# Kernel optimization log

Hardware: AMD Instinct MI355X
Metric: run time of the kernel (lower is better)

Reference implementation:

```python
import jax, jax.numpy as jnp
import numpy as np

K = 3  # neighborhood kernel size (hard-coded by the view(B,H,W,3,3) in the source)
BIG_NEG = jnp.float32(-1e9)   # stand-in for -inf on masked neighbors (safe under softmax)
ROW_NEG = jnp.float32(-1e8)   # value used by the source for fully-occluded rows


def extract_local_patches(x, k=K):
    """x: [B,C,H,W] -> [B,C,H,W,k*k] with replicate padding (F.pad mode='replicate')."""
    p = k // 2
    xp = jnp.pad(x, ((0, 0), (0, 0), (p, p), (p, p)), mode='edge')
    B, C, H, W = x.shape
    shifts = [xp[:, :, i:i + H, j:j + W] for i in range(k) for j in range(k)]
    return jnp.stack(shifts, axis=-1)  # [B,C,H,W,k*k]


def setup_inputs() -> dict:
    key = jax.random.key(0)
    k1, k2, k3, k4 = jax.random.split(key, 4)
    B, C, H, W = 4, 640, 64, 64
    Ft = jax.random.normal(k1, (B, C, H, W), dtype=jnp.float32)
    Fwarp = jax.random.normal(k2, (B, C, H, W), dtype=jnp.float32)
    mask = jax.random.bernoulli(k3, 0.3, (B, 1, H, W)).astype(jnp.float32)
    conv_w = jax.random.normal(k4, (1, 2 * C), dtype=jnp.float32) * (1.0 / np.sqrt(2 * C))
    conv_b = jnp.zeros((1,), dtype=jnp.float32)
    return {"Ft": Ft, "Fwarp": Fwarp, "mask": mask, "conv_w": conv_w, "conv_b": conv_b}


def reference(Ft, Fwarp, mask, conv_w, conv_b):
    B, C, H, W = Ft.shape
    # 3x3 neighborhood of Fwarp: [B,C,H,W,9]
    Fp = extract_local_patches(Fwarp)
    # per-pixel dot product of Ft query with each of its 9 neighbors
    sim = jnp.einsum('bchw,bchwn->bhwn', Ft, Fp) / jnp.sqrt(jnp.float32(C))  # [B,H,W,9]
    # mask neighborhoods: [B,H,W,9]
    mp = extract_local_patches(mask)[:, 0]
    occluded = (mp == 1.0)
    sim = jnp.where(occluded, BIG_NEG, sim)
    # rows where every neighbor is occluded get a uniform large-negative row,
    # softmax'd then zeroed (matches masked_fill(-inf) -> -1e8 -> zero-out)
    valid = jnp.any(~occluded, axis=-1, keepdims=True)  # [B,H,W,1]
    sim = jnp.where(valid, sim, ROW_NEG)
    attn = jax.nn.softmax(sim, axis=-1)
    attn = jnp.where(valid, attn, 0.0)  # [B,H,W,9]
    # weighted sum over the 9 neighbors
    Fw = jnp.einsum('bchwn,bhwn->bchw', Fp, attn)  # [B,C,H,W]
    # lambda predictor: 1x1 conv + sigmoid over cat([Fwarp_weighted, Ft])
    x = jnp.concatenate([Fw, Ft], axis=1)  # [B,2C,H,W]
    lam = jax.nn.sigmoid(jnp.einsum('bihw,oi->bohw', x, conv_w) + conv_b[None, :, None, None])
    return lam * Ft + (1.0 - lam) * Fw
```

## Files before the change

kernel.cpp:

```cpp
#include <hip/hip_runtime.h>

#define B_    4
#define C_    640
#define H_    64
#define W_    64
#define NT    512
#define G_    8
#define CPG   40
#define CHALF 320

__device__ __forceinline__ void decode_bhs(int n, int& b, int& h, int& s) {
    const int xcd = n & 7;
    const int i   = n >> 3;
    h = xcd * 8 + (i & 7);
    s = (i >> 3) & 1;
    b = i >> 4;
}

__device__ __forceinline__ void row_acc(const float4 ft4, const float4 r,
                                        const int l16, float* a) {
    const float pw = __shfl_up(r.w, 1, 64);
    const float nx = __shfl_down(r.x, 1, 64);
    const float vL0 = (l16 == 0)  ? r.x : pw;
    const float vR3 = (l16 == 15) ? r.w : nx;
    a[0]  = fmaf(ft4.x, vL0, a[0]);
    a[1]  = fmaf(ft4.y, r.x, a[1]);
    a[2]  = fmaf(ft4.z, r.y, a[2]);
    a[3]  = fmaf(ft4.w, r.z, a[3]);
    a[4]  = fmaf(ft4.x, r.x, a[4]);
    a[5]  = fmaf(ft4.y, r.y, a[5]);
    a[6]  = fmaf(ft4.z, r.z, a[6]);
    a[7]  = fmaf(ft4.w, r.w, a[7]);
    a[8]  = fmaf(ft4.x, r.y, a[8]);
    a[9]  = fmaf(ft4.y, r.z, a[9]);
    a[10] = fmaf(ft4.z, r.w, a[10]);
    a[11] = fmaf(ft4.w, vR3, a[11]);
}

__device__ __forceinline__ void row_fw(const float4 r, const int l16,
                                       const float* at, const int r3, float* fwv) {
    const float pw = __shfl_up(r.w, 1, 64);
    const float nx = __shfl_down(r.x, 1, 64);
    const float vL0 = (l16 == 0)  ? r.x : pw;
    const float vR3 = (l16 == 15) ? r.w : nx;
    fwv[0] += at[0*9+r3]*vL0 + at[0*9+r3+1]*r.x + at[0*9+r3+2]*r.y;
    fwv[1] += at[1*9+r3]*r.x + at[1*9+r3+1]*r.y + at[1*9+r3+2]*r.z;
    fwv[2] += at[2*9+r3]*r.y + at[2*9+r3+1]*r.z + at[2*9+r3+2]*r.w;
    fwv[3] += at[3*9+r3]*r.z + at[3*9+r3+1]*r.w + at[3*9+r3+2]*vR3;
}

__global__ __launch_bounds__(NT, 4) void k1_sim(
    const float* __restrict__ Ft, const float* __restrict__ Fwp,
    const float* __restrict__ cw,
    float* __restrict__ simp, float* __restrict__ ptp)
{
    __shared__ float lds_cw[2 * C_];
    __shared__ float lds_sim[G_][W_][9];
    __shared__ float lds_PT[G_][4][W_];

    const int t   = threadIdx.x;
    const int l   = t & 63;
    const int g   = t >> 6;
    const int sub = l >> 4;
    const int l16 = l & 15;
    const int w0  = l16 * 4;

    int b, h, s; decode_bhs(blockIdx.x, b, h, s);
    const int hm = (h > 0) ? h - 1 : 0;
    const int hp = (h < H_ - 1) ? h + 1 : H_ - 1;
    const size_t cs = (size_t)H_ * W_;
    const int c0 = s * CHALF + g * CPG;

    for (int i = t; i < 2 * C_; i += NT) lds_cw[i] = cw[i];
    __syncthreads();

    const size_t base = (size_t)(b * C_ + c0) * H_;
    const size_t lo   = (size_t)sub * cs + w0;
    const float* ftp = Ft  + (base + h ) * W_ + lo;
    const float* q0p = Fwp + (base + hm) * W_ + lo;
    const float* q1p = Fwp + (base + h ) * W_ + lo;
    const float* q2p = Fwp + (base + hp) * W_ + lo;

    float acc[36], Pp[12], T4[4];
    #pragma unroll
    for (int i = 0; i < 36; ++i) acc[i] = 0.f;
    #pragma unroll
    for (int i = 0; i < 12; ++i) Pp[i] = 0.f;
    #pragma unroll
    for (int i = 0; i < 4; ++i) T4[i] = 0.f;

    #pragma unroll 2
    for (int k = 0; k < CPG; k += 4) {
        const size_t off = (size_t)k * cs;
        const float4 ft4 = *(const float4*)(ftp + off);
        const float4 r0  = *(const float4*)(q0p + off);
        const float4 r1  = *(const float4*)(q1p + off);
        const float4 r2  = *(const float4*)(q2p + off);
        row_acc(ft4, r0, l16, &acc[0]);
        row_acc(ft4, r1, l16, &acc[12]);
        row_acc(ft4, r2, l16, &acc[24]);
        const int c = c0 + k + sub;
        const float wF = lds_cw[c];
        const float wT = lds_cw[C_ + c];
        Pp[0] = fmaf(wF, r0.x, Pp[0]); Pp[1]  = fmaf(wF, r0.y, Pp[1]);
        Pp[2] = fmaf(wF, r0.z, Pp[2]); Pp[3]  = fmaf(wF, r0.w, Pp[3]);
        Pp[4] = fmaf(wF, r1.x, Pp[4]); Pp[5]  = fmaf(wF, r1.y, Pp[5]);
        Pp[6] = fmaf(wF, r1.z, Pp[6]); Pp[7]  = fmaf(wF, r1.w, Pp[7]);
        Pp[8] = fmaf(wF, r2.x, Pp[8]); Pp[9]  = fmaf(wF, r2.y, Pp[9]);
        Pp[10]= fmaf(wF, r2.z, Pp[10]);Pp[11] = fmaf(wF, r2.w, Pp[11]);
        T4[0] = fmaf(wT, ft4.x, T4[0]); T4[1] = fmaf(wT, ft4.y, T4[1]);
        T4[2] = fmaf(wT, ft4.z, T4[2]); T4[3] = fmaf(wT, ft4.w, T4[3]);
    }

    #pragma unroll
    for (int i = 0; i < 36; ++i) {
        acc[i] += __shfl_xor(acc[i], 16, 64);
        acc[i] += __shfl_xor(acc[i], 32, 64);
    }
    #pragma unroll
    for (int i = 0; i < 12; ++i) {
        Pp[i] += __shfl_xor(Pp[i], 16, 64);
        Pp[i] += __shfl_xor(Pp[i], 32, 64);
    }
    #pragma unroll
    for (int i = 0; i < 4; ++i) {
        T4[i] += __shfl_xor(T4[i], 16, 64);
        T4[i] += __shfl_xor(T4[i], 32, 64);
    }

    if (l < 16) {
        #pragma unroll
        for (int px = 0; px < 4; ++px) {
            #pragma unroll
            for (int r = 0; r < 3; ++r) {
                #pragma unroll
                for (int cc = 0; cc < 3; ++cc)
                    lds_sim[g][w0 + px][r * 3 + cc] = acc[r * 12 + cc * 4 + px];
                lds_PT[g][r][w0 + px] = Pp[r * 4 + px];
            }
            lds_PT[g][3][w0 + px] = T4[px];
        }
    }
    __syncthreads();

    const size_t r2i = (size_t)((b * H_ + h) * 2 + s);
    float* sp = simp + r2i * (W_ * 9);
    for (int idx = t; idx < W_ * 9; idx += NT) {
        const int ww = idx / 9, q = idx % 9;
        float v = 0.f;
        #pragma unroll
        for (int gg = 0; gg < G_; ++gg) v += lds_sim[gg][ww][q];
        sp[idx] = v;
    }
    if (t < 4 * W_) {
        const int r = t >> 6, ww = t & 63;
        float v = 0.f;
        #pragma unroll
        for (int gg = 0; gg < G_; ++gg) v += lds_PT[gg][r][ww];
        ptp[r2i * (4 * W_) + t] = v;
    }
}

__global__ __launch_bounds__(NT, 4) void k2_out(
    const float* __restrict__ Ft, const float* __restrict__ Fwp,
    const float* __restrict__ mask, const float* __restrict__ cb,
    const float* __restrict__ simp, const float* __restrict__ ptp,
    float* __restrict__ out)
{
    __shared__ float lds_msk[3][W_];
    __shared__ float lds_attn[W_][9];
    __shared__ float lds_Pf[4][W_];
    __shared__ float lds_lam[W_];

    const int t   = threadIdx.x;
    const int l   = t & 63;
    const int g   = t >> 6;
    const int sub = l >> 4;
    const int l16 = l & 15;
    const int w0  = l16 * 4;

    int b, h, s; decode_bhs(blockIdx.x, b, h, s);
    const int hm = (h > 0) ? h - 1 : 0;
    const int hp = (h < H_ - 1) ? h + 1 : H_ - 1;
    const size_t cs = (size_t)H_ * W_;
    const int c0 = s * CHALF + g * CPG;

    if (t < 3 * W_) {
        const int r = t >> 6, col = t & 63;
        const int row = (r == 0) ? hm : ((r == 1) ? h : hp);
        lds_msk[r][col] = mask[((size_t)b * H_ + row) * W_ + col];
    }
    __syncthreads();

    const size_t bh2 = (size_t)((b * H_ + h) * 2);
    const float* sp0 = simp + (bh2 + 0) * (W_ * 9);
    const float* sp1 = simp + (bh2 + 1) * (W_ * 9);
    for (int idx = t; idx < W_ * 9; idx += NT) {
        const int ww = idx / 9, q = idx % 9;
        float v = (sp0[idx] + sp1[idx]) * 0.03952847075210474f;
        const int r = q / 3, j = q % 3;
        int col = ww + j - 1;
        col = col < 0 ? 0 : (col > W_ - 1 ? W_ - 1 : col);
        if (lds_msk[r][col] == 1.0f) v = -1e9f;
        lds_attn[ww][q] = v;
    }
    if (t < 4 * W_) {
        lds_Pf[t >> 6][t & 63] =
            ptp[(bh2 + 0) * (4 * W_) + t] + ptp[(bh2 + 1) * (4 * W_) + t];
    }
    __syncthreads();

    if (t < W_) {
        float v[9];
        float mx = -3e38f;
        bool valid = false;
        #pragma unroll
        for (int q = 0; q < 9; ++q) {
            v[q] = lds_attn[t][q];
            if (v[q] > -5e8f) valid = true;
            mx = fmaxf(mx, v[q]);
        }
        float a9[9];
        if (!valid) {
            #pragma unroll
            for (int q = 0; q < 9; ++q) a9[q] = 0.f;
        } else {
            float sum = 0.f;
            #pragma unroll
            for (int q = 0; q < 9; ++q) { a9[q] = expf(v[q] - mx); sum += a9[q]; }
            const float inv = 1.f / sum;
            #pragma unroll
            for (int q = 0; q < 9; ++q) a9[q] *= inv;
        }
        #pragma unroll
        for (int q = 0; q < 9; ++q) lds_attn[t][q] = a9[q];

        float lamF = 0.f;
        #pragma unroll
        for (int r = 0; r < 3; ++r)
            #pragma unroll
            for (int j = 0; j < 3; ++j) {
                int col = t + j - 1;
                col = col < 0 ? 0 : (col > W_ - 1 ? W_ - 1 : col);
                lamF = fmaf(a9[r * 3 + j], lds_Pf[r][col], lamF);
            }
        const float d = lds_Pf[3][t] + lamF + cb[0];
        lds_lam[t] = 1.f / (1.f + expf(-d));
    }
    __syncthreads();

    float at[36];
    #pragma unroll
    for (int px = 0; px < 4; ++px)
        #pragma unroll
        for (int q = 0; q < 9; ++q) at[px * 9 + q] = lds_attn[w0 + px][q];
    float lam4[4], oml4[4];
    #pragma unroll
    for (int px = 0; px < 4; ++px) {
        lam4[px] = lds_lam[w0 + px];
        oml4[px] = 1.f - lam4[px];
    }

    const size_t base = (size_t)(b * C_ + c0) * H_;
    const size_t lo   = (size_t)sub * cs + w0;
    const float* ftp = Ft  + (base + h ) * W_ + lo;
    const float* q0p = Fwp + (base + hm) * W_ + lo;
    const float* q1p = Fwp + (base + h ) * W_ + lo;
    const float* q2p = Fwp + (base + hp) * W_ + lo;
    float* outp = out + (base + h) * W_ + lo;

    #pragma unroll 2
    for (int k = 0; k < CPG; k += 4) {
        const size_t off = (size_t)k * cs;
        const float4 ft4 = *(const float4*)(ftp + off);
        const float4 r0  = *(const float4*)(q0p + off);
        const float4 r1  = *(const float4*)(q1p + off);
        const float4 r2  = *(const float4*)(q2p + off);
        float fwv[4] = {0.f, 0.f, 0.f, 0.f};
        row_fw(r0, l16, at, 0, fwv);
        row_fw(r1, l16, at, 3, fwv);
        row_fw(r2, l16, at, 6, fwv);
        float4 o;
        o.x = lam4[0] * ft4.x + oml4[0] * fwv[0];
        o.y = lam4[1] * ft4.y + oml4[1] * fwv[1];
        o.z = lam4[2] * ft4.z + oml4[2] * fwv[2];
        o.w = lam4[3] * ft4.w + oml4[3] * fwv[3];
        *(float4*)(outp + off) = o;
    }
}

extern "C" void kernel_launch(void* const* d_in, const int* in_sizes, int n_in,
                              void* d_out, int out_size, void* d_ws, size_t ws_size,
                              hipStream_t stream) {
    const float* Ft   = (const float*)d_in[0];
    const float* Fwp  = (const float*)d_in[1];
    const float* mask = (const float*)d_in[2];
    const float* cw   = (const float*)d_in[3];
    const float* cb   = (const float*)d_in[4];
    float* out = (float*)d_out;

    float* simp = (float*)d_ws;
    float* ptp  = simp + (size_t)512 * (W_ * 9);

    dim3 grid(B_ * H_ * 2);
    dim3 block(NT);
    k1_sim<<<grid, block, 0, stream>>>(Ft, Fwp, cw, simp, ptp);
    k2_out<<<grid, block, 0, stream>>>(Ft, Fwp, mask, cb, simp, ptp, out);
}
```

Measured before the change: 47.60 us.

## Fuse similarity and output kernels with per-row atomic flag handshake

Merges the two kernels into one. The two blocks that handle a (b,h) row's channel halves exchange partial similarity sums through global memory, guarded by a per-row atomic counter and a spin-wait. This drops one kernel launch and lets the second phase reuse the Ft/Fwarp pointers, with the data likely still in cache. In exchange it adds a memset launch and 19KB of dynamic shared memory that is requested but never used, which may lower occupancy. The spin-wait deadlocks unless both partner blocks are resident at the same time, which holds only because the grid of 512 blocks fits on the device.

```diff
diff --git a/kernel.cpp b/kernel.cpp
--- a/kernel.cpp
+++ b/kernel.cpp
@@ -49,14 +49,20 @@
     fwv[3] += at[3*9+r3]*r.z + at[3*9+r3+1]*r.w + at[3*9+r3+2]*vR3;
 }
 
-__global__ __launch_bounds__(NT, 4) void k1_sim(
+__global__ __launch_bounds__(NT, 4) void nca_persist(
     const float* __restrict__ Ft, const float* __restrict__ Fwp,
-    const float* __restrict__ cw,
-    float* __restrict__ simp, float* __restrict__ ptp)
+    const float* __restrict__ mask,
+    const float* __restrict__ cw, const float* __restrict__ cb,
+    int* __restrict__ flags, float* __restrict__ simp, float* __restrict__ ptp,
+    float* __restrict__ out)
 {
     __shared__ float lds_cw[2 * C_];
+    __shared__ float lds_msk[3][W_];
     __shared__ float lds_sim[G_][W_][9];
     __shared__ float lds_PT[G_][4][W_];
+    __shared__ float lds_attn[W_][9];
+    __shared__ float lds_Pf[4][W_];
+    __shared__ float lds_lam[W_];
 
     const int t   = threadIdx.x;
     const int l   = t & 63;
@@ -66,12 +72,18 @@
     const int w0  = l16 * 4;
 
     int b, h, s; decode_bhs(blockIdx.x, b, h, s);
+    const int rowid = b * H_ + h;
     const int hm = (h > 0) ? h - 1 : 0;
     const int hp = (h < H_ - 1) ? h + 1 : H_ - 1;
     const size_t cs = (size_t)H_ * W_;
     const int c0 = s * CHALF + g * CPG;
 
     for (int i = t; i < 2 * C_; i += NT) lds_cw[i] = cw[i];
+    if (t < 3 * W_) {
+        const int r = t >> 6, col = t & 63;
+        const int row = (r == 0) ? hm : ((r == 1) ? h : hp);
+        lds_msk[r][col] = mask[((size_t)b * H_ + row) * W_ + col];
+    }
     __syncthreads();
 
     const size_t base = (size_t)(b * C_ + c0) * H_;
@@ -143,7 +155,7 @@
     }
     __syncthreads();
 
-    const size_t r2i = (size_t)((b * H_ + h) * 2 + s);
+    const size_t r2i = (size_t)(rowid * 2 + s);
     float* sp = simp + r2i * (W_ * 9);
     for (int idx = t; idx < W_ * 9; idx += NT) {
         const int ww = idx / 9, q = idx % 9;
@@ -159,40 +171,19 @@
         for (int gg = 0; gg < G_; ++gg) v += lds_PT[gg][r][ww];
         ptp[r2i * (4 * W_) + t] = v;
     }
-}
-
-__global__ __launch_bounds__(NT, 4) void k2_out(
-    const float* __restrict__ Ft, const float* __restrict__ Fwp,
-    const float* __restrict__ mask, const float* __restrict__ cb,
-    const float* __restrict__ simp, const float* __restrict__ ptp,
-    float* __restrict__ out)
-{
-    __shared__ float lds_msk[3][W_];
-    __shared__ float lds_attn[W_][9];
-    __shared__ float lds_Pf[4][W_];
-    __shared__ float lds_lam[W_];
-
-    const int t   = threadIdx.x;
-    const int l   = t & 63;
-    const int g   = t >> 6;
-    const int sub = l >> 4;
-    const int l16 = l & 15;
-    const int w0  = l16 * 4;
-
-    int b, h, s; decode_bhs(blockIdx.x, b, h, s);
-    const int hm = (h > 0) ? h - 1 : 0;
-    const int hp = (h < H_ - 1) ? h + 1 : H_ - 1;
-    const size_t cs = (size_t)H_ * W_;
-    const int c0 = s * CHALF + g * CPG;
-
-    if (t < 3 * W_) {
-        const int r = t >> 6, col = t & 63;
-        const int row = (r == 0) ? hm : ((r == 1) ? h : hp);
-        lds_msk[r][col] = mask[((size_t)b * H_ + row) * W_ + col];
-    }
-    __syncthreads();
-
-    const size_t bh2 = (size_t)((b * H_ + h) * 2);
+
+    __threadfence();
+    __syncthreads();
+    if (t == 0) {
+        atomicAdd(&flags[rowid], 1);
+        while (atomicAdd(&flags[rowid], 0) < 2) {
+            __builtin_amdgcn_s_sleep(2);
+        }
+        __threadfence();
+    }
+    __syncthreads();
+
+    const size_t bh2 = (size_t)(rowid * 2);
     const float* sp0 = simp + (bh2 + 0) * (W_ * 9);
     const float* sp1 = simp + (bh2 + 1) * (W_ * 9);
     for (int idx = t; idx < W_ * 9; idx += NT) {
@@ -261,14 +252,7 @@
         oml4[px] = 1.f - lam4[px];
     }
 
-    const size_t base = (size_t)(b * C_ + c0) * H_;
-    const size_t lo   = (size_t)sub * cs + w0;
-    const float* ftp = Ft  + (base + h ) * W_ + lo;
-    const float* q0p = Fwp + (base + hm) * W_ + lo;
-    const float* q1p = Fwp + (base + h ) * W_ + lo;
-    const float* q2p = Fwp + (base + hp) * W_ + lo;
     float* outp = out + (base + h) * W_ + lo;
-
     #pragma unroll 2
     for (int k = 0; k < CPG; k += 4) {
         const size_t off = (size_t)k * cs;
@@ -299,11 +283,14 @@
     const float* cb   = (const float*)d_in[4];
     float* out = (float*)d_out;
 
-    float* simp = (float*)d_ws;
-    float* ptp  = simp + (size_t)512 * (W_ * 9);
+    int*   flags = (int*)d_ws;
+    float* simp  = (float*)((char*)d_ws + 1024);
+    float* ptp   = simp + (size_t)512 * (W_ * 9);
+
+    hipMemsetAsync(d_ws, 0, 1024, stream);
 
     dim3 grid(B_ * H_ * 2);
     dim3 block(NT);
-    k1_sim<<<grid, block, 0, stream>>>(Ft, Fwp, cw, simp, ptp);
-    k2_out<<<grid, block, 0, stream>>>(Ft, Fwp, mask, cb, simp, ptp, out);
-}
+    nca_persist<<<grid, block, 19 * 1024, stream>>>(
+        Ft, Fwp, mask, cw, cb, flags, simp, ptp, out);
+}
```

Result: slower. 130.8 us (+174.9%).

## Fuse two kernels into one cooperative launch with grid-wide barrier

Applied to the files above, without the earlier changes.

Merges the similarity pass and the output pass into a single cooperative kernel separated by a grid sync, so the gap between two launches disappears and the same blocks reread their input rows while they may still sit in cache. Mask and conv weights are loaded once at the start. The fused kernel uses more shared memory and the grid barrier costs time, which can reduce occupancy. If the cooperative launch fails, the code falls back to the two original kernels.

```diff
diff --git a/kernel.cpp b/kernel.cpp
--- a/kernel.cpp
+++ b/kernel.cpp
@@ -1,4 +1,7 @@
 #include <hip/hip_runtime.h>
+#include <hip/hip_cooperative_groups.h>
+
+namespace cg = cooperative_groups;
 
 #define B_    4
 #define C_    640
@@ -49,38 +52,12 @@
     fwv[3] += at[3*9+r3]*r.z + at[3*9+r3+1]*r.w + at[3*9+r3+2]*vR3;
 }
 
-__global__ __launch_bounds__(NT, 4) void k1_sim(
-    const float* __restrict__ Ft, const float* __restrict__ Fwp,
-    const float* __restrict__ cw,
-    float* __restrict__ simp, float* __restrict__ ptp)
-{
-    __shared__ float lds_cw[2 * C_];
-    __shared__ float lds_sim[G_][W_][9];
-    __shared__ float lds_PT[G_][4][W_];
-
-    const int t   = threadIdx.x;
-    const int l   = t & 63;
-    const int g   = t >> 6;
-    const int sub = l >> 4;
-    const int l16 = l & 15;
-    const int w0  = l16 * 4;
-
-    int b, h, s; decode_bhs(blockIdx.x, b, h, s);
-    const int hm = (h > 0) ? h - 1 : 0;
-    const int hp = (h < H_ - 1) ? h + 1 : H_ - 1;
-    const size_t cs = (size_t)H_ * W_;
-    const int c0 = s * CHALF + g * CPG;
-
-    for (int i = t; i < 2 * C_; i += NT) lds_cw[i] = cw[i];
-    __syncthreads();
-
-    const size_t base = (size_t)(b * C_ + c0) * H_;
-    const size_t lo   = (size_t)sub * cs + w0;
-    const float* ftp = Ft  + (base + h ) * W_ + lo;
-    const float* q0p = Fwp + (base + hm) * W_ + lo;
-    const float* q1p = Fwp + (base + h ) * W_ + lo;
-    const float* q2p = Fwp + (base + hp) * W_ + lo;
-
+__device__ __forceinline__ void phase1_stream(
+    const float* ftp, const float* q0p, const float* q1p, const float* q2p,
+    const float* lds_cw, int c0, int sub, int l, int l16, int g, int w0, int t,
+    float (*lds_sim)[W_][9], float (*lds_PT)[4][W_],
+    float* simp, float* ptp, size_t r2i, size_t cs)
+{
     float acc[36], Pp[12], T4[4];
     #pragma unroll
     for (int i = 0; i < 36; ++i) acc[i] = 0.f;
@@ -143,7 +120,6 @@
     }
     __syncthreads();
 
-    const size_t r2i = (size_t)((b * H_ + h) * 2 + s);
     float* sp = simp + r2i * (W_ * 9);
     for (int idx = t; idx < W_ * 9; idx += NT) {
         const int ww = idx / 9, q = idx % 9;
@@ -161,38 +137,12 @@
     }
 }
 
-__global__ __launch_bounds__(NT, 4) void k2_out(
-    const float* __restrict__ Ft, const float* __restrict__ Fwp,
-    const float* __restrict__ mask, const float* __restrict__ cb,
-    const float* __restrict__ simp, const float* __restrict__ ptp,
-    float* __restrict__ out)
-{
-    __shared__ float lds_msk[3][W_];
-    __shared__ float lds_attn[W_][9];
-    __shared__ float lds_Pf[4][W_];
-    __shared__ float lds_lam[W_];
-
-    const int t   = threadIdx.x;
-    const int l   = t & 63;
-    const int g   = t >> 6;
-    const int sub = l >> 4;
-    const int l16 = l & 15;
-    const int w0  = l16 * 4;
-
-    int b, h, s; decode_bhs(blockIdx.x, b, h, s);
-    const int hm = (h > 0) ? h - 1 : 0;
-    const int hp = (h < H_ - 1) ? h + 1 : H_ - 1;
-    const size_t cs = (size_t)H_ * W_;
-    const int c0 = s * CHALF + g * CPG;
-
-    if (t < 3 * W_) {
-        const int r = t >> 6, col = t & 63;
-        const int row = (r == 0) ? hm : ((r == 1) ? h : hp);
-        lds_msk[r][col] = mask[((size_t)b * H_ + row) * W_ + col];
-    }
-    __syncthreads();
-
-    const size_t bh2 = (size_t)((b * H_ + h) * 2);
+__device__ __forceinline__ void phase2_out(
+    const float* ftp, const float* q0p, const float* q1p, const float* q2p,
+    float* outp, const float* simp, const float* ptp, const float* cb,
+    const float (*lds_msk)[W_], float (*lds_attn)[9], float (*lds_Pf)[W_],
+    float* lds_lam, int t, int l16, int w0, size_t bh2, size_t cs)
+{
     const float* sp0 = simp + (bh2 + 0) * (W_ * 9);
     const float* sp1 = simp + (bh2 + 1) * (W_ * 9);
     for (int idx = t; idx < W_ * 9; idx += NT) {
@@ -260,14 +210,6 @@
         lam4[px] = lds_lam[w0 + px];
         oml4[px] = 1.f - lam4[px];
     }
-
-    const size_t base = (size_t)(b * C_ + c0) * H_;
-    const size_t lo   = (size_t)sub * cs + w0;
-    const float* ftp = Ft  + (base + h ) * W_ + lo;
-    const float* q0p = Fwp + (base + hm) * W_ + lo;
-    const float* q1p = Fwp + (base + h ) * W_ + lo;
-    const float* q2p = Fwp + (base + hp) * W_ + lo;
-    float* outp = out + (base + h) * W_ + lo;
 
     #pragma unroll 2
     for (int k = 0; k < CPG; k += 4) {
@@ -289,6 +231,125 @@
     }
 }
 
+__global__ __launch_bounds__(NT, 4) void nca_coop(
+    const float* __restrict__ Ft, const float* __restrict__ Fwp,
+    const float* __restrict__ mask,
+    const float* __restrict__ cw, const float* __restrict__ cb,
+    float* __restrict__ simp, float* __restrict__ ptp,
+    float* __restrict__ out)
+{
+    __shared__ float lds_cw[2 * C_];
+    __shared__ float lds_msk[3][W_];
+    __shared__ float lds_sim[G_][W_][9];
+    __shared__ float lds_PT[G_][4][W_];
+    __shared__ float lds_attn[W_][9];
+    __shared__ float lds_Pf[4][W_];
+    __shared__ float lds_lam[W_];
+
+    const int t   = threadIdx.x;
+    const int l   = t & 63;
+    const int g   = t >> 6;
+    const int sub = l >> 4;
+    const int l16 = l & 15;
+    const int w0  = l16 * 4;
+
+    int b, h, s; decode_bhs(blockIdx.x, b, h, s);
+    const int rowid = b * H_ + h;
+    const int hm = (h > 0) ? h - 1 : 0;
+    const int hp = (h < H_ - 1) ? h + 1 : H_ - 1;
+    const size_t cs = (size_t)H_ * W_;
+    const int c0 = s * CHALF + g * CPG;
+
+    for (int i = t; i < 2 * C_; i += NT) lds_cw[i] = cw[i];
+    if (t < 3 * W_) {
+        const int r = t >> 6, col = t & 63;
+        const int row = (r == 0) ? hm : ((r == 1) ? h : hp);
+        lds_msk[r][col] = mask[((size_t)b * H_ + row) * W_ + col];
+    }
+    __syncthreads();
+
+    const size_t base = (size_t)(b * C_ + c0) * H_;
+    const size_t lo   = (size_t)sub * cs + w0;
+    const float* ftp = Ft  + (base + h ) * W_ + lo;
+    const float* q0p = Fwp + (base + hm) * W_ + lo;
+    const float* q1p = Fwp + (base + h ) * W_ + lo;
+    const float* q2p = Fwp + (base + hp) * W_ + lo;
+
+    phase1_stream(ftp, q0p, q1p, q2p, lds_cw, c0, sub, l, l16, g, w0, t,
+                  lds_sim, lds_PT, simp, ptp, (size_t)(rowid * 2 + s), cs);
+
+    __threadfence();
+    cg::this_grid().sync();
+
+    phase2_out(ftp, q0p, q1p, q2p, out + (base + h) * W_ + lo,
+               simp, ptp, cb, lds_msk, lds_attn, lds_Pf, lds_lam,
+               t, l16, w0, (size_t)(rowid * 2), cs);
+}
+
+__global__ __launch_bounds__(NT, 4) void k1_sim(
+    const float* __restrict__ Ft, const float* __restrict__ Fwp,
+    const float* __restrict__ cw,
+    float* __restrict__ simp, float* __restrict__ ptp)
+{
+    __shared__ float lds_cw[2 * C_];
+    __shared__ float lds_sim[G_][W_][9];
+    __shared__ float lds_PT[G_][4][W_];
+
+    const int t = threadIdx.x, l = t & 63, g = t >> 6;
+    const int sub = l >> 4, l16 = l & 15, w0 = l16 * 4;
+    int b, h, s; decode_bhs(blockIdx.x, b, h, s);
+    const int hm = (h > 0) ? h - 1 : 0;
+    const int hp = (h < H_ - 1) ? h + 1 : H_ - 1;
+    const size_t cs = (size_t)H_ * W_;
+    const int c0 = s * CHALF + g * CPG;
+
+    for (int i = t; i < 2 * C_; i += NT) lds_cw[i] = cw[i];
+    __syncthreads();
+
+    const size_t base = (size_t)(b * C_ + c0) * H_;
+    const size_t lo   = (size_t)sub * cs + w0;
+    phase1_stream(Ft + (base + h) * W_ + lo, Fwp + (base + hm) * W_ + lo,
+                  Fwp + (base + h) * W_ + lo, Fwp + (base + hp) * W_ + lo,
+                  lds_cw, c0, sub, l, l16, g, w0, t,
+                  lds_sim, lds_PT, simp, ptp,
+                  (size_t)((b * H_ + h) * 2 + s), cs);
+}
+
+__global__ __launch_bounds__(NT, 4) void k2_out(
+    const float* __restrict__ Ft, const float* __restrict__ Fwp,
+    const float* __restrict__ mask, const float* __restrict__ cb,
+    const float* __restrict__ simp, const float* __restrict__ ptp,
+    float* __restrict__ out)
+{
+    __shared__ float lds_msk[3][W_];
+    __shared__ float lds_attn[W_][9];
+    __shared__ float lds_Pf[4][W_];
+    __shared__ float lds_lam[W_];
+
+    const int t = threadIdx.x, l = t & 63, g = t >> 6;
+    const int sub = l >> 4, l16 = l & 15, w0 = l16 * 4;
+    int b, h, s; decode_bhs(blockIdx.x, b, h, s);
+    const int hm = (h > 0) ? h - 1 : 0;
+    const int hp = (h < H_ - 1) ? h + 1 : H_ - 1;
+    const size_t cs = (size_t)H_ * W_;
+    const int c0 = s * CHALF + g * CPG;
+
+    if (t < 3 * W_) {
+        const int r = t >> 6, col = t & 63;
+        const int row = (r == 0) ? hm : ((r == 1) ? h : hp);
+        lds_msk[r][col] = mask[((size_t)b * H_ + row) * W_ + col];
+    }
+    __syncthreads();
+
+    const size_t base = (size_t)(b * C_ + c0) * H_;
+    const size_t lo   = (size_t)sub * cs + w0;
+    phase2_out(Ft + (base + h) * W_ + lo, Fwp + (base + hm) * W_ + lo,
+               Fwp + (base + h) * W_ + lo, Fwp + (base + hp) * W_ + lo,
+               out + (base + h) * W_ + lo, simp, ptp, cb,
+               lds_msk, lds_attn, lds_Pf, lds_lam,
+               t, l16, w0, (size_t)((b * H_ + h) * 2), cs);
+}
+
 extern "C" void kernel_launch(void* const* d_in, const int* in_sizes, int n_in,
                               void* d_out, int out_size, void* d_ws, size_t ws_size,
                               hipStream_t stream) {
@@ -304,6 +365,13 @@
 
     dim3 grid(B_ * H_ * 2);
     dim3 block(NT);
-    k1_sim<<<grid, block, 0, stream>>>(Ft, Fwp, cw, simp, ptp);
-    k2_out<<<grid, block, 0, stream>>>(Ft, Fwp, mask, cb, simp, ptp, out);
-}
+
+    void* args[] = {(void*)&Ft, (void*)&Fwp, (void*)&mask, (void*)&cw,
+                    (void*)&cb, (void*)&simp, (void*)&ptp, (void*)&out};
+    hipError_t err = hipLaunchCooperativeKernel((void*)nca_coop, grid, block,
+                                                args, 0, stream);
+    if (err != hipSuccess) {
+        k1_sim<<<grid, block, 0, stream>>>(Ft, Fwp, cw, simp, ptp);
+        k2_out<<<grid, block, 0, stream>>>(Ft, Fwp, mask, cb, simp, ptp, out);
+    }
+}
```

After: 165.8 us. +248.3%, slower.
